# Kernel tuning notes

Hardware: AMD Instinct MI355X
Metric: run time of the kernel (lower is better)

## Reference

```python
import jax, jax.numpy as jnp
import numpy as np

N_WAY = 100
K_SHOT = 10
N_SUPPORT = N_WAY * K_SHOT
N_QUERY = 8192
F_IN = 4096
D_EMB = 1024
EPS = 1e-6  # torch nn.PairwiseDistance default eps added to the difference


def setup_inputs() -> dict:
    key = jax.random.key(0)
    k1, k2, k3, k4 = jax.random.split(key, 4)
    support_images = jax.random.normal(k1, (N_SUPPORT, F_IN), dtype=jnp.float32)
    # dense labels 0..N_WAY-1, K_SHOT examples each (episodic sampling)
    support_labels = (jnp.arange(N_SUPPORT, dtype=jnp.int32) // K_SHOT)
    query_images = jax.random.normal(k2, (N_QUERY, F_IN), dtype=jnp.float32)
    W = jax.random.normal(k3, (F_IN, D_EMB), dtype=jnp.float32) * (1.0 / np.sqrt(F_IN))
    b = jax.random.normal(k4, (D_EMB,), dtype=jnp.float32) * 0.01
    return {"support_images": support_images, "support_labels": support_labels,
            "query_images": query_images, "W": W, "b": b}


def reference(support_images, support_labels, query_images, W, b):
    # backbone: linear feature extractor
    z_support = support_images @ W + b          # [N_SUPPORT, D]
    z_query = query_images @ W + b              # [N_QUERY, D]

    # group support embeddings by class (each class has exactly K_SHOT members)
    order = jnp.argsort(support_labels, stable=True)
    grouped = z_support[order].reshape(N_WAY, K_SHOT, D_EMB)  # [W, K, D]

    # torch .median(dim=0): lower median for even counts -> sorted[(K-1)//2]
    z_proto_med = jnp.sort(grouped, axis=1)[:, (K_SHOT - 1) // 2]  # [W, D]
    z_proto_mean = grouped.mean(axis=1)                            # [W, D]
    z_total = 0.5 * (z_proto_med + z_proto_mean)                   # [W, D]

    # pairwise L2 with torch PairwiseDistance eps: sqrt(sum((q - p + eps)^2))
    # expanded: ||q||^2 + ||p||^2 + D*eps^2 - 2 q.p + 2*eps*(sum q - sum p)
    q2 = jnp.sum(z_query * z_query, axis=-1, keepdims=True)       # [Q, 1]
    p2 = jnp.sum(z_total * z_total, axis=-1)[None, :]             # [1, W]
    qs = jnp.sum(z_query, axis=-1, keepdims=True)                 # [Q, 1]
    ps = jnp.sum(z_total, axis=-1)[None, :]                       # [1, W]
    cross = z_query @ z_total.T                                   # [Q, W]
    sq = q2 + p2 - 2.0 * cross + 2.0 * EPS * (qs - ps) + D_EMB * EPS * EPS
    dists = jnp.sqrt(jnp.maximum(sq, 0.0))                        # [Q, W]
    return -dists
```

## Files before the change

kernel.cpp:

```cpp
#include <hip/hip_runtime.h>


typedef unsigned short u16;
typedef __attribute__((ext_vector_type(4))) unsigned short u16x4;
typedef __attribute__((ext_vector_type(8))) unsigned short u16x8;
typedef __attribute__((ext_vector_type(8))) short bf16x8;
typedef __attribute__((ext_vector_type(4))) float f32x4;

#define N_QUERY 8192
#define F_IN    4096
#define D_EMB   1024
#define N_SUP   1000
#define N_WAY   100
#define BK      64
#define BM      96

__device__ __forceinline__ u16 f2b(float f) {
  unsigned int u = __builtin_bit_cast(unsigned int, f);
  u += 0x7FFFu + ((u >> 16) & 1u);
  return (u16)(u >> 16);
}
__device__ __forceinline__ float b2f(u16 u) {
  unsigned int x = ((unsigned int)u) << 16;
  return __builtin_bit_cast(float, x);
}

#define GLB_PTR(p) ((const __attribute__((address_space(1))) unsigned int*)(p))
#define LDS_PTR(p) ((__attribute__((address_space(3))) unsigned int*)(p))

__global__ __launch_bounds__(256) void wt_k(const float* __restrict__ W,
                                            u16* __restrict__ Wt) {
  __shared__ float tile[32][33];
  int kb = blockIdx.x * 32, nb = blockIdx.y * 32;
  int tx = threadIdx.x & 31, ty = threadIdx.x >> 5;
#pragma unroll
  for (int i = 0; i < 4; ++i) {
    int k = ty + i * 8;
    tile[k][tx] = W[(size_t)(kb + k) * D_EMB + nb + tx];
  }
  __syncthreads();
#pragma unroll
  for (int i = 0; i < 4; ++i) {
    int n = ty + i * 8;
    Wt[(size_t)(nb + n) * F_IN + kb + tx] = f2b(tile[tx][n]);
  }
}

__global__ __launch_bounds__(512) void gemm1_k(
    const float* __restrict__ qimg, const float* __restrict__ simg,
    const u16* __restrict__ Wt, const float* __restrict__ bias,
    u16* __restrict__ Zq) {
  __shared__ __align__(16) u16 As[BM * BK];
  __shared__ __align__(16) u16 Bs[128 * BK];
  const int tid  = threadIdx.x;
  const int lane = tid & 63, wid = tid >> 6;
  const int wr = wid >> 2, wc = wid & 3;
  int lin = blockIdx.x + (blockIdx.y << 3);
  int swz = (lin & 7) * 96 + (lin >> 3);
  const int rowBase = (swz >> 3) * BM;
  const int colBase = (swz & 7) * 128;
  const bool a2 = (tid < 256);

  const float* asrc[2];
  int aw[2];
#pragma unroll
  for (int i = 0; i < 2; ++i) {
    int g = i * 512 + tid;
    if (g > 767) g = 767;
    int row = g >> 3;
    int colb = ((g & 7) << 4) ^ ((row & 7) << 4);
    int grow = rowBase + row;
    int sr = grow - N_QUERY; if (sr < 0) sr = 0; if (sr > N_SUP - 1) sr = N_SUP - 1;
    const float* base = (grow < N_QUERY) ? qimg + (size_t)grow * F_IN
                                         : simg + (size_t)sr * F_IN;
    asrc[i] = base + (colb >> 1);
    aw[i] = g * 8;
  }
  const u16* bsrc[2];
  unsigned bldsoff[2];
#pragma unroll
  for (int i = 0; i < 2; ++i) {
    int g = i * 512 + tid;
    int n = g >> 3;
    int kb = ((g & 7) << 4) ^ ((n & 7) << 4);
    bsrc[i] = Wt + (size_t)(colBase + n) * F_IN + (kb >> 1);
    bldsoff[i] = i * 8192 + wid * 1024;
  }
  int aoff[3], boff[2];
#pragma unroll
  for (int m = 0; m < 3; ++m) {
    int row = wr * 48 + m * 16 + (lane & 15);
    aoff[m] = (row * 128 + (((lane >> 4) << 4) ^ ((row & 7) << 4))) >> 1;
  }
#pragma unroll
  for (int n = 0; n < 2; ++n) {
    int row = wc * 32 + n * 16 + (lane & 15);
    boff[n] = (row * 128 + (((lane >> 4) << 4) ^ ((row & 7) << 4))) >> 1;
  }

  f32x4 acc[3][2] = {};

#pragma unroll 1
  for (int kt = 0; kt < F_IN / BK; ++kt) {
    float4 v0a = *(const float4*)(asrc[0] + kt * BK);
    float4 v0b = *(const float4*)(asrc[0] + kt * BK + 4);
    float4 v1a = {}, v1b = {};
    if (a2) {
      v1a = *(const float4*)(asrc[1] + kt * BK);
      v1b = *(const float4*)(asrc[1] + kt * BK + 4);
    }
#pragma unroll
    for (int i = 0; i < 2; ++i)
      __builtin_amdgcn_global_load_lds(GLB_PTR(bsrc[i] + kt * BK),
                                       LDS_PTR((char*)Bs + bldsoff[i]), 16, 0, 0);
    u16x8 pk0 = { f2b(v0a.x), f2b(v0a.y), f2b(v0a.z), f2b(v0a.w),
                  f2b(v0b.x), f2b(v0b.y), f2b(v0b.z), f2b(v0b.w) };
    *(u16x8*)&As[aw[0]] = pk0;
    if (a2) {
      u16x8 pk1 = { f2b(v1a.x), f2b(v1a.y), f2b(v1a.z), f2b(v1a.w),
                    f2b(v1b.x), f2b(v1b.y), f2b(v1b.z), f2b(v1b.w) };
      *(u16x8*)&As[aw[1]] = pk1;
    }
    __syncthreads();

#pragma unroll
    for (int ks = 0; ks < 2; ++ks) {
      bf16x8 a[3], b[2];
#pragma unroll
      for (int m = 0; m < 3; ++m) a[m] = *(const bf16x8*)&As[aoff[m] ^ (ks << 5)];
#pragma unroll
      for (int n = 0; n < 2; ++n) b[n] = *(const bf16x8*)&Bs[boff[n] ^ (ks << 5)];
#pragma unroll
      for (int m = 0; m < 3; ++m)
#pragma unroll
        for (int n = 0; n < 2; ++n)
          acc[m][n] = __builtin_amdgcn_mfma_f32_16x16x32_bf16(a[m], b[n], acc[m][n], 0, 0, 0);
    }
    __syncthreads();
  }

#pragma unroll
  for (int n = 0; n < 2; ++n) {
    int c = colBase + wc * 32 + n * 16 + (lane & 15);
    float bvv = bias[c];
#pragma unroll
    for (int m = 0; m < 3; ++m) {
      int r0 = rowBase + wr * 48 + m * 16 + ((lane >> 4) * 4);
#pragma unroll
      for (int r = 0; r < 4; ++r)
        Zq[(size_t)(r0 + r) * D_EMB + c] = f2b(acc[m][n][r] + bvv);
    }
  }
}

__global__ __launch_bounds__(256) void proto_k(const u16* __restrict__ Zq,
                                               float* __restrict__ Ztf) {
  int gid = blockIdx.x * 256 + threadIdx.x;
  int w = gid >> 10, d = gid & 1023;
  float outv = 0.f;
  if (w < N_WAY) {
    float v[10]; float s = 0.f;
#pragma unroll
    for (int k = 0; k < 10; ++k) {
      v[k] = b2f(Zq[(size_t)(N_QUERY + w * 10 + k) * D_EMB + d]);
      s += v[k];
    }
#pragma unroll
    for (int a = 0; a < 9; ++a)
#pragma unroll
      for (int b2 = 0; b2 < 9; ++b2)
        if (b2 < 9 - a) {
          float lo = fminf(v[b2], v[b2 + 1]);
          float hi = fmaxf(v[b2], v[b2 + 1]);
          v[b2] = lo; v[b2 + 1] = hi;
        }
    outv = 0.5f * (v[4] + s * 0.1f);
  }
  Ztf[gid] = outv;
}

__global__ __launch_bounds__(256) void stats_k(const float* __restrict__ in,
                                               u16* __restrict__ outb,
                                               float* __restrict__ sum2,
                                               float* __restrict__ sum1) {
  int row = blockIdx.x;
  const float* r = in + (size_t)row * D_EMB;
  int t = threadIdx.x;
  float4 v = *(const float4*)(r + t * 4);
  u16x4 u4 = { f2b(v.x), f2b(v.y), f2b(v.z), f2b(v.w) };
  *(u16x4*)(outb + (size_t)row * D_EMB + t * 4) = u4;
  float s  = v.x + v.y + v.z + v.w;
  float s2 = v.x * v.x + v.y * v.y + v.z * v.z + v.w * v.w;
#pragma unroll
  for (int off = 32; off > 0; off >>= 1) {
    s  += __shfl_down(s, off);
    s2 += __shfl_down(s2, off);
  }
  __shared__ float as1[4], as2[4];
  if ((t & 63) == 0) { as1[t >> 6] = s; as2[t >> 6] = s2; }
  __syncthreads();
  if (t == 0) {
    sum1[row] = as1[0] + as1[1] + as1[2] + as1[3];
    sum2[row] = as2[0] + as2[1] + as2[2] + as2[3];
  }
}

#define LDA2 40
__global__ __launch_bounds__(256) void gemm2_k(
    const u16* __restrict__ Zq, const u16* __restrict__ Ztb,
    const float* __restrict__ p2, const float* __restrict__ ps,
    float* __restrict__ out) {
  __shared__ u16 As[32][LDA2];
  __shared__ u16 Bs[128][LDA2];
  __shared__ float q2_l[32], qs_l[32];
  const int tid = threadIdx.x;
  const int lane = tid & 63, wid = tid >> 6;
  const int wr = wid >> 1, wc = wid & 1;
  const int rowBase = blockIdx.x * 32;
  const bool stA = (tid < 128);

  f32x4 acc[4] = {};
  float rs = 0.f, rs2 = 0.f;

  for (int kt = 0; kt < D_EMB / 32; ++kt) {
    u16x8 avv = {};
    if (stA) {
      int row = tid >> 2, kh = tid & 3;
      avv = *(const u16x8*)(Zq + (size_t)(rowBase + row) * D_EMB + kt * 32 + kh * 8);
    }
    u16x8 bvv[2];
#pragma unroll
    for (int i = 0; i < 2; ++i) {
      int u = i * 256 + tid;
      int n = u >> 2, kh = u & 3;
      bvv[i] = *(const u16x8*)(Ztb + (size_t)n * D_EMB + kt * 32 + kh * 8);
    }
    __syncthreads();
    if (stA) {
      int row = tid >> 2, kh = tid & 3;
      *(u16x8*)&As[row][kh * 8] = avv;
#pragma unroll
      for (int j = 0; j < 8; ++j) {
        float x = b2f(avv[j]);
        rs += x; rs2 += x * x;
      }
    }
#pragma unroll
    for (int i = 0; i < 2; ++i) {
      int u = i * 256 + tid;
      int n = u >> 2, kh = u & 3;
      *(u16x8*)&Bs[n][kh * 8] = bvv[i];
    }
    __syncthreads();

    bf16x8 a, b[4];
    a = *(const bf16x8*)&As[wr * 16 + (lane & 15)][(lane >> 4) * 8];
#pragma unroll
    for (int n = 0; n < 4; ++n)
      b[n] = *(const bf16x8*)&Bs[wc * 64 + n * 16 + (lane & 15)][(lane >> 4) * 8];
#pragma unroll
    for (int n = 0; n < 4; ++n)
      acc[n] = __builtin_amdgcn_mfma_f32_16x16x32_bf16(a, b[n], acc[n], 0, 0, 0);
    __syncthreads();
  }

  rs  += __shfl_down(rs, 1);  rs  += __shfl_down(rs, 2);
  rs2 += __shfl_down(rs2, 1); rs2 += __shfl_down(rs2, 2);
  if (stA && (tid & 3) == 0) {
    qs_l[tid >> 2] = rs;
    q2_l[tid >> 2] = rs2;
  }
  __syncthreads();

  {
    int r0 = wr * 16 + ((lane >> 4) * 4);
    float q2v[4], qsv[4];
#pragma unroll
    for (int r = 0; r < 4; ++r) { q2v[r] = q2_l[r0 + r]; qsv[r] = qs_l[r0 + r]; }
#pragma unroll
    for (int n = 0; n < 4; ++n) {
      int c = wc * 64 + n * 16 + (lane & 15);
      if (c < N_WAY) {
        float pp = p2[c], pss = ps[c];
#pragma unroll
        for (int r = 0; r < 4; ++r) {
          float sq = q2v[r] + pp - 2.f * acc[n][r]
                   + 2e-6f * (qsv[r] - pss) + (float)D_EMB * 1e-12f;
          out[(size_t)(rowBase + r0 + r) * N_WAY + c] = -sqrtf(fmaxf(sq, 0.f));
        }
      }
    }
  }
}

extern "C" void kernel_launch(void* const* d_in, const int* in_sizes, int n_in,
                              void* d_out, int out_size, void* d_ws, size_t ws_size,
                              hipStream_t stream) {
  const float* simg = (const float*)d_in[0];
  const float* qimg = (const float*)d_in[2];
  const float* W    = (const float*)d_in[3];
  const float* bias = (const float*)d_in[4];
  float* out = (float*)d_out;

  char* ws = (char*)d_ws;
  u16*   Wt  = (u16*)(ws);
  u16*   Zq  = (u16*)(ws + 8388608);
  float* Ztf = (float*)(ws + 27262976);
  u16*   Ztb = (u16*)(ws + 27787264);
  float* p2  = (float*)(ws + 28114944);
  float* ps  = (float*)(ws + 28115456);

  hipLaunchKernelGGL(wt_k,    dim3(128, 32), dim3(256), 0, stream, W, Wt);
  hipLaunchKernelGGL(gemm1_k, dim3(8, 96),   dim3(512), 0, stream, qimg, simg, Wt, bias, Zq);
  hipLaunchKernelGGL(proto_k, dim3(512),     dim3(256), 0, stream, Zq, Ztf);
  hipLaunchKernelGGL(stats_k, dim3(128),     dim3(256), 0, stream, Ztf, Ztb, p2, ps);
  hipLaunchKernelGGL(gemm2_k, dim3(256),     dim3(256), 0, stream, Zq, Ztb, p2, ps, out);
}
```

Baseline: 139.2 us.

## Software-pipeline A-tile global loads one k-step ahead in gemm1

Restructures the gemm1 main loop so the fp32 A-tile loads for step k+1 are issued before converting and storing step k, using double-buffered registers, manual waitcnt and sched_barriers. The A loading is rebalanced so all 512 threads each load three float4 chunks instead of a divergent split with two float4 pairs. Adds a launch-bounds occupancy hint of 6. The aim is to hide global load latency behind MFMA work, at the cost of more registers and reliance on hand-tuned vmcnt counts.

```diff
diff --git a/kernel.cpp b/kernel.cpp
--- a/kernel.cpp
+++ b/kernel.cpp
@@ -27,6 +27,7 @@
 
 #define GLB_PTR(p) ((const __attribute__((address_space(1))) unsigned int*)(p))
 #define LDS_PTR(p) ((__attribute__((address_space(3))) unsigned int*)(p))
+#define SB() __builtin_amdgcn_sched_barrier(0)
 
 __global__ __launch_bounds__(256) void wt_k(const float* __restrict__ W,
                                             u16* __restrict__ Wt) {
@@ -46,7 +47,7 @@
   }
 }
 
-__global__ __launch_bounds__(512) void gemm1_k(
+__global__ __launch_bounds__(512, 6) void gemm1_k(
     const float* __restrict__ qimg, const float* __restrict__ simg,
     const u16* __restrict__ Wt, const float* __restrict__ bias,
     u16* __restrict__ Zq) {
@@ -59,22 +60,20 @@
   int swz = (lin & 7) * 96 + (lin >> 3);
   const int rowBase = (swz >> 3) * BM;
   const int colBase = (swz & 7) * 128;
-  const bool a2 = (tid < 256);
-
-  const float* asrc[2];
-  int aw[2];
-#pragma unroll
-  for (int i = 0; i < 2; ++i) {
-    int g = i * 512 + tid;
-    if (g > 767) g = 767;
-    int row = g >> 3;
-    int colb = ((g & 7) << 4) ^ ((row & 7) << 4);
+
+  const float* asrc[3];
+  int aw[3];
+#pragma unroll
+  for (int j = 0; j < 3; ++j) {
+    int hc = j * 512 + tid;
+    int row = hc >> 4, w = hc & 15;
+    int colb = (w * 8) ^ ((row & 7) << 4);
     int grow = rowBase + row;
     int sr = grow - N_QUERY; if (sr < 0) sr = 0; if (sr > N_SUP - 1) sr = N_SUP - 1;
     const float* base = (grow < N_QUERY) ? qimg + (size_t)grow * F_IN
                                          : simg + (size_t)sr * F_IN;
-    asrc[i] = base + (colb >> 1);
-    aw[i] = g * 8;
+    asrc[j] = base + (colb >> 1);
+    aw[j] = hc * 4;
   }
   const u16* bsrc[2];
   unsigned bldsoff[2];
@@ -99,45 +98,81 @@
   }
 
   f32x4 acc[3][2] = {};
+  float4 aE[3], aO[3];
+
+#define LOAD_A(REG, KT)                                                        \
+  { REG[0] = *(const float4*)(asrc[0] + (KT) * BK);                            \
+    REG[1] = *(const float4*)(asrc[1] + (KT) * BK);                            \
+    REG[2] = *(const float4*)(asrc[2] + (KT) * BK); }
+
+#define STAGE_B(KT)                                                            \
+  { _Pragma("unroll")                                                          \
+    for (int i_ = 0; i_ < 2; ++i_)                                             \
+      __builtin_amdgcn_global_load_lds(GLB_PTR(bsrc[i_] + (KT) * BK),          \
+          LDS_PTR((char*)Bs + bldsoff[i_]), 16, 0, 0); }
+
+#define CVT_A(REG)                                                             \
+  { _Pragma("unroll")                                                          \
+    for (int j_ = 0; j_ < 3; ++j_) {                                           \
+      u16x4 pk_ = { f2b(REG[j_].x), f2b(REG[j_].y),                            \
+                    f2b(REG[j_].z), f2b(REG[j_].w) };                          \
+      *(u16x4*)&As[aw[j_]] = pk_;                                              \
+    } }
+
+#define COMPUTE()                                                              \
+  { _Pragma("unroll")                                                          \
+    for (int ks = 0; ks < 2; ++ks) {                                           \
+      bf16x8 a_[3], b_[2];                                                     \
+      _Pragma("unroll")                                                        \
+      for (int m = 0; m < 3; ++m)                                              \
+        a_[m] = *(const bf16x8*)&As[aoff[m] ^ (ks << 5)];                      \
+      _Pragma("unroll")                                                        \
+      for (int n = 0; n < 2; ++n)                                              \
+        b_[n] = *(const bf16x8*)&Bs[boff[n] ^ (ks << 5)];                      \
+      _Pragma("unroll")                                                        \
+      for (int m = 0; m < 3; ++m)                                              \
+        _Pragma("unroll")                                                      \
+        for (int n = 0; n < 2; ++n)                                            \
+          acc[m][n] = __builtin_amdgcn_mfma_f32_16x16x32_bf16(a_[m], b_[n],    \
+                                                              acc[m][n], 0, 0, 0); } }
+
+#define ITER(T, RC, RN)                                                        \
+  {                                                                            \
+    STAGE_B(T);                                                                \
+    SB();                                                                      \
+    LOAD_A(RN, (T) + 1);                                                       \
+    SB();                                                                      \
+    CVT_A(RC);                                                                 \
+    asm volatile("s_waitcnt vmcnt(3) lgkmcnt(0)" ::: "memory");                \
+    __builtin_amdgcn_s_barrier();                                              \
+    SB();                                                                      \
+    COMPUTE();                                                                 \
+    __builtin_amdgcn_s_barrier();                                              \
+    SB();                                                                      \
+  }
+
+  LOAD_A(aE, 0);
+  SB();
 
 #pragma unroll 1
-  for (int kt = 0; kt < F_IN / BK; ++kt) {
-    float4 v0a = *(const float4*)(asrc[0] + kt * BK);
-    float4 v0b = *(const float4*)(asrc[0] + kt * BK + 4);
-    float4 v1a = {}, v1b = {};
-    if (a2) {
-      v1a = *(const float4*)(asrc[1] + kt * BK);
-      v1b = *(const float4*)(asrc[1] + kt * BK + 4);
-    }
-#pragma unroll
-    for (int i = 0; i < 2; ++i)
-      __builtin_amdgcn_global_load_lds(GLB_PTR(bsrc[i] + kt * BK),
-                                       LDS_PTR((char*)Bs + bldsoff[i]), 16, 0, 0);
-    u16x8 pk0 = { f2b(v0a.x), f2b(v0a.y), f2b(v0a.z), f2b(v0a.w),
-                  f2b(v0b.x), f2b(v0b.y), f2b(v0b.z), f2b(v0b.w) };
-    *(u16x8*)&As[aw[0]] = pk0;
-    if (a2) {
-      u16x8 pk1 = { f2b(v1a.x), f2b(v1a.y), f2b(v1a.z), f2b(v1a.w),
-                    f2b(v1b.x), f2b(v1b.y), f2b(v1b.z), f2b(v1b.w) };
-      *(u16x8*)&As[aw[1]] = pk1;
-    }
-    __syncthreads();
-
-#pragma unroll
-    for (int ks = 0; ks < 2; ++ks) {
-      bf16x8 a[3], b[2];
-#pragma unroll
-      for (int m = 0; m < 3; ++m) a[m] = *(const bf16x8*)&As[aoff[m] ^ (ks << 5)];
-#pragma unroll
-      for (int n = 0; n < 2; ++n) b[n] = *(const bf16x8*)&Bs[boff[n] ^ (ks << 5)];
-#pragma unroll
-      for (int m = 0; m < 3; ++m)
-#pragma unroll
-        for (int n = 0; n < 2; ++n)
-          acc[m][n] = __builtin_amdgcn_mfma_f32_16x16x32_bf16(a[m], b[n], acc[m][n], 0, 0, 0);
-    }
-    __syncthreads();
-  }
+  for (int t2 = 0; t2 < 31; ++t2) {
+    ITER(2 * t2,     aE, aO);
+    ITER(2 * t2 + 1, aO, aE);
+  }
+  ITER(62, aE, aO);
+  STAGE_B(63);
+  SB();
+  CVT_A(aO);
+  asm volatile("s_waitcnt vmcnt(0) lgkmcnt(0)" ::: "memory");
+  __builtin_amdgcn_s_barrier();
+  SB();
+  COMPUTE();
+
+#undef ITER
+#undef COMPUTE
+#undef CVT_A
+#undef STAGE_B
+#undef LOAD_A
 
 #pragma unroll
   for (int n = 0; n < 2; ++n) {
```

Result: slower. 148.0 us, median of 2 (+6.3%).
